# Kernel tuning notes

Hardware: AMD Instinct MI355X
Metric: run time of the kernel (lower is better)

The kernel has to match this reference:

```python
import jax, jax.numpy as jnp
import numpy as np

B, C, H, W = 4, 256, 64, 64
HID = max(C // 8, 64)  # = 64


def setup_inputs() -> dict:
    key = jax.random.key(0)
    ks = jax.random.split(key, 8)
    s_in = 1.0 / np.sqrt(C)
    return {
        "x1": jax.random.normal(ks[0], (B, C, H, W), dtype=jnp.float32),
        "x2": jax.random.normal(ks[1], (B, C, H, W), dtype=jnp.float32),
        "Wq": jax.random.normal(ks[2], (HID, C), dtype=jnp.float32) * s_in,
        "bq": jnp.zeros((HID,), dtype=jnp.float32),
        "Wk": jax.random.normal(ks[3], (HID, C), dtype=jnp.float32) * s_in,
        "bk": jnp.zeros((HID,), dtype=jnp.float32),
        "Wv": jax.random.normal(ks[4], (C, C), dtype=jnp.float32) * s_in,
        "bv": jnp.zeros((C,), dtype=jnp.float32),
        "gamma": jnp.ones((1,), dtype=jnp.float32) * 0.5,  # nonzero so attention path matters
    }


def _conv1x1(x, Wt, b):
    # 1x1 conv == per-pixel GEMM: (O,C) x (B,C,H,W) -> (B,O,H,W)
    return jnp.einsum("oc,bchw->bohw", Wt, x) + b[None, :, None, None]


def _cross_attend(xq, xkv, Wq, bq, Wk, bk, Wv, bv, gamma):
    b, c, h, w = xq.shape
    n = h * w
    q = _conv1x1(xq, Wq, bq).reshape(b, -1, n)    # (B, hid, N)
    k = _conv1x1(xkv, Wk, bk).reshape(b, -1, n)   # (B, hid, N)
    v = _conv1x1(xkv, Wv, bv).reshape(b, c, n)    # (B, C, N)
    # attn[b,n,m] = softmax_m( q[:, :, n] . k[:, :, m] )
    attn = jax.nn.softmax(jnp.einsum("bhn,bhm->bnm", q, k), axis=-1)
    out = jnp.einsum("bcm,bnm->bcn", v, attn).reshape(b, c, h, w)
    return xq + gamma[0] * out


def reference(x1, x2, Wq, bq, Wk, bk, Wv, bv, gamma):
    x1_att = _cross_attend(x1, x2, Wq, bq, Wk, bk, Wv, bv, gamma)
    x2_att = _cross_attend(x2, x1, Wq, bq, Wk, bk, Wv, bv, gamma)
    return (x1_att, x2_att)
```

## Files before the change

kernel.cpp:

```cpp
#include <hip/hip_runtime.h>
#include <hip/hip_bf16.h>

#define NPIX 4096
#define CCH  256
#define HID  64
#define BAT  4
#define XSTR 264
#define PTS  136


using f32x4 = __attribute__((ext_vector_type(4))) float;
using h16x8 = __attribute__((ext_vector_type(8))) _Float16;
using u16x4 = __attribute__((ext_vector_type(4))) unsigned short;

#define L2E 1.44269504088896340736f

__device__ __forceinline__ unsigned short f2h(float f) {
    _Float16 h = (_Float16)f;
    return __builtin_bit_cast(unsigned short, h);
}
__device__ __forceinline__ h16x8 ldg_fragh(const unsigned short* p) {
    uint4 v = *reinterpret_cast<const uint4*>(p);
    return __builtin_bit_cast(h16x8, v);
}
__device__ __forceinline__ h16x8 lds_fragh(const unsigned short* p) {
    return *reinterpret_cast<const h16x8*>(p);
}
__device__ __forceinline__ unsigned int pk2h(float a, float b) {
    auto t = __builtin_amdgcn_cvt_pkrtz(a, b);
    return __builtin_bit_cast(unsigned int, t);
}
__device__ __forceinline__ float sel4(float a0, float a1, float a2, float a3, int q) {
    float x = (q & 1) ? a1 : a0;
    float y = (q & 1) ? a3 : a2;
    return (q & 2) ? y : x;
}

__global__ __launch_bounds__(256, 1) void wcvt_kernel(
    const float* __restrict__ Wq, const float* __restrict__ Wk,
    const float* __restrict__ Wv, unsigned short* __restrict__ Wg)
{
    int tid = blockIdx.x * 256 + threadIdx.x;
    int tile = tid >> 6, lane = tid & 63;
    int r = (tile >> 3) * 16 + (lane & 15);
    int c = (tile & 7) * 32 + (lane >> 4) * 8;
    const float* src; float sc;
    if (r < 64)       { src = Wq + r * CCH + c;        sc = L2E; }
    else if (r < 128) { src = Wk + (r - 64) * CCH + c; sc = 1.0f; }
    else              { src = Wv + (r - 128) * CCH + c; sc = 1.0f; }
    float4 a = *reinterpret_cast<const float4*>(src);
    float4 b4 = *reinterpret_cast<const float4*>(src + 4);
    uint4 out;
    out.x = pk2h(a.x * sc, a.y * sc);
    out.y = pk2h(a.z * sc, a.w * sc);
    out.z = pk2h(b4.x * sc, b4.y * sc);
    out.w = pk2h(b4.z * sc, b4.w * sc);
    *reinterpret_cast<uint4*>(Wg + tile * 512 + lane * 8) = out;
}

__global__ __launch_bounds__(256, 2) void proj_kernel(
    const float* __restrict__ x1, const float* __restrict__ x2,
    const unsigned short* __restrict__ Wg,
    const float* __restrict__ bq, const float* __restrict__ bk,
    const float* __restrict__ bv,
    unsigned short* __restrict__ Qf, unsigned short* __restrict__ Kf,
    unsigned short* __restrict__ Vt)
{
    __shared__ unsigned short xs[32][XSTR];

    const int Lb = blockIdx.x;
    const int sb = Lb & 7;
    const int tile = Lb >> 3;
    const int s = sb >> 2, b = sb & 3;
    const float* x = s ? x2 : x1;
    const int n0 = tile * 32;
    const int t = threadIdx.x;
    const int lane = t & 63;
    const int w = __builtin_amdgcn_readfirstlane(t >> 6);
    const int quad = lane >> 4, lq = lane & 15;

    {
        const int n = t & 31;
        const int g = t >> 5;
        const float* xb = x + (size_t)(b * CCH) * NPIX + n0;
        #pragma unroll
        for (int i = 0; i < 8; ++i) {
            int c0 = g * 4 + i * 32;
            u16x4 hv;
            #pragma unroll
            for (int j = 0; j < 4; ++j)
                hv[j] = f2h(xb[(size_t)(c0 + j) * NPIX + n]);
            *reinterpret_cast<u16x4*>(&xs[n][c0]) = hv;
        }
    }
    __syncthreads();

    h16x8 xf[2][8];
    #pragma unroll
    for (int nt = 0; nt < 2; ++nt)
        #pragma unroll
        for (int ks = 0; ks < 8; ++ks)
            xf[nt][ks] = lds_fragh(&xs[nt * 16 + lq][ks * 32 + quad * 8]);

    unsigned short* Qb = Qf + (size_t)(s * BAT + b) * (NPIX * HID);
    unsigned short* Kb = Kf + (size_t)(s * BAT + b) * (NPIX * HID);
    unsigned short* Vb = Vt + (size_t)(s * BAT + b) * ((size_t)CCH * NPIX);

    h16x8 wf[2][8];
    {
        const unsigned short* wp = Wg + (size_t)(w * 6 * 8) * 512 + lane * 8;
        #pragma unroll
        for (int ks = 0; ks < 8; ++ks) wf[0][ks] = ldg_fragh(wp + ks * 512);
    }

    #pragma unroll
    for (int hloop = 0; hloop < 6; ++hloop) {
        const int cur = hloop & 1;
        const int idx = w * 6 + hloop;
        const int kind = idx < 4 ? 0 : (idx < 8 ? 1 : 2);

        if (hloop < 5) {
            const unsigned short* wp = Wg + (size_t)((idx + 1) * 8) * 512 + lane * 8;
            #pragma unroll
            for (int ks = 0; ks < 8; ++ks) wf[cur ^ 1][ks] = ldg_fragh(wp + ks * 512);
        }

        if (kind == 2) {
            const int cbase = (idx - 8) * 16;
            const float bbv = bv[cbase + lq];
            #pragma unroll
            for (int nt = 0; nt < 2; ++nt) {
                f32x4 acc = (f32x4){0.f, 0.f, 0.f, 0.f};
                #pragma unroll
                for (int ks = 0; ks < 8; ++ks)
                    acc = __builtin_amdgcn_mfma_f32_16x16x32_f16(xf[nt][ks], wf[cur][ks], acc, 0, 0, 0);
                u16x4 pk;
                #pragma unroll
                for (int reg = 0; reg < 4; ++reg) pk[reg] = f2h(acc[reg] + bbv);
                size_t off = (size_t)((idx - 8) * 128 + (n0 >> 5)) * 512
                           + (nt * 2 + (quad >> 1)) * 128 + lq * 8 + (quad & 1) * 4;
                *reinterpret_cast<unsigned long long*>(Vb + off) =
                    __builtin_bit_cast(unsigned long long, pk);
            }
        } else {
            unsigned short* dq = (kind ? Kb : Qb);
            const float* bias = (kind ? bk : bq);
            const float scl = kind ? 1.0f : L2E;
            const int hb16 = kind ? (idx - 4) : idx;
            float bb4[4];
            #pragma unroll
            for (int reg = 0; reg < 4; ++reg)
                bb4[reg] = bias[hb16 * 16 + quad * 4 + reg] * scl;
            #pragma unroll
            for (int nt = 0; nt < 2; ++nt) {
                f32x4 acc = (f32x4){0.f, 0.f, 0.f, 0.f};
                #pragma unroll
                for (int ks = 0; ks < 8; ++ks)
                    acc = __builtin_amdgcn_mfma_f32_16x16x32_f16(wf[cur][ks], xf[nt][ks], acc, 0, 0, 0);
                u16x4 pk;
                #pragma unroll
                for (int reg = 0; reg < 4; ++reg) pk[reg] = f2h(acc[reg] + bb4[reg]);
                size_t off = (size_t)((n0 >> 4) + nt) * 1024 + (hb16 >> 1) * 512
                           + ((hb16 & 1) * 2 + (quad >> 1)) * 128 + lq * 8 + (quad & 1) * 4;
                *reinterpret_cast<unsigned long long*>(dq + off) =
                    __builtin_bit_cast(unsigned long long, pk);
            }
        }
    }
}

__global__ __launch_bounds__(256, 2) void smax_kernel(
    const unsigned short* __restrict__ Qf, const unsigned short* __restrict__ Kf,
    float* __restrict__ Mg)
{
    __shared__ float Msh[4][64];

    const int Lb = blockIdx.x;
    const int g = Lb & 7;
    const int ntile = Lb >> 3;
    const int d = g >> 2, b = g & 3;
    const int db = d * BAT + b;
    const int s = d, r = 1 - d;
    const int n0 = ntile * 64;

    const int t = threadIdx.x;
    const int lane = t & 63;
    const int w = __builtin_amdgcn_readfirstlane(t >> 6);
    const int quad = lane >> 4, lq = lane & 15;

    const unsigned short* Qb = Qf + (size_t)(s * BAT + b) * (NPIX * HID);
    const unsigned short* Kb = Kf + (size_t)(r * BAT + b) * (NPIX * HID);

    h16x8 qf[4][2];
    #pragma unroll
    for (int nt = 0; nt < 4; ++nt)
        #pragma unroll
        for (int ks = 0; ks < 2; ++ks)
            qf[nt][ks] = ldg_fragh(Qb + (size_t)((((n0 >> 4) + nt) * 2) + ks) * 512 + lane * 8);

    float mx[4] = {-3.0e38f, -3.0e38f, -3.0e38f, -3.0e38f};

    h16x8 kfA[2][2], kfB[2][2];

#define SMAX_LOAD(BUF, IT)                                                      \
    {                                                                           \
        _Pragma("unroll")                                                       \
        for (int mt = 0; mt < 2; ++mt) {                                        \
            _Pragma("unroll")                                                   \
            for (int ks = 0; ks < 2; ++ks)                                      \
                BUF[mt][ks] = ldg_fragh(                                        \
                    Kb + (size_t)(((IT) * 8 + w * 2 + mt) * 2 + ks) * 512       \
                       + lane * 8);                                             \
        }                                                                       \
    }
#define SMAX_STEP(BUF)                                                          \
    {                                                                           \
        f32x4 Sacc[2][4];                                                       \
        _Pragma("unroll")                                                       \
        for (int mt = 0; mt < 2; ++mt) {                                        \
            _Pragma("unroll")                                                   \
            for (int nt = 0; nt < 4; ++nt)                                      \
                Sacc[mt][nt] = (f32x4){0.f, 0.f, 0.f, 0.f};                     \
        }                                                                       \
        _Pragma("unroll")                                                       \
        for (int mt = 0; mt < 2; ++mt) {                                        \
            _Pragma("unroll")                                                   \
            for (int ks = 0; ks < 2; ++ks) {                                    \
                _Pragma("unroll")                                               \
                for (int nt = 0; nt < 4; ++nt)                                  \
                    Sacc[mt][nt] = __builtin_amdgcn_mfma_f32_16x16x32_f16(      \
                        BUF[mt][ks], qf[nt][ks], Sacc[mt][nt], 0, 0, 0);        \
            }                                                                   \
        }                                                                       \
        _Pragma("unroll")                                                       \
        for (int mt = 0; mt < 2; ++mt) {                                        \
            _Pragma("unroll")                                                   \
            for (int nt = 0; nt < 4; ++nt)                                      \
                mx[nt] = fmaxf(mx[nt],                                          \
                    fmaxf(fmaxf(Sacc[mt][nt][0], Sacc[mt][nt][1]),              \
                          fmaxf(Sacc[mt][nt][2], Sacc[mt][nt][3])));            \
        }                                                                       \
    }

    SMAX_LOAD(kfA, 0)
    for (int it = 0; it < 32; it += 2) {
        if (it + 1 < 32) SMAX_LOAD(kfB, it + 1)
        SMAX_STEP(kfA)
        if (it + 2 < 32) SMAX_LOAD(kfA, it + 2)
        SMAX_STEP(kfB)
    }
#undef SMAX_LOAD
#undef SMAX_STEP

    #pragma unroll
    for (int nt = 0; nt < 4; ++nt) {
        mx[nt] = fmaxf(mx[nt], __shfl_xor(mx[nt], 16));
        mx[nt] = fmaxf(mx[nt], __shfl_xor(mx[nt], 32));
    }
    Msh[w][quad * 16 + lq] = sel4(mx[0], mx[1], mx[2], mx[3], quad);
    __syncthreads();

    if (t < 64) {
        float m = fmaxf(fmaxf(Msh[0][t], Msh[1][t]), fmaxf(Msh[2][t], Msh[3][t]));
        Mg[(size_t)db * NPIX + n0 + t] = m;
    }
}

__global__ __launch_bounds__(256, 2) void attn_kernel(
    const float* __restrict__ x1, const float* __restrict__ x2,
    const unsigned short* __restrict__ Qf, const unsigned short* __restrict__ Kf,
    const unsigned short* __restrict__ Vt,
    const float* __restrict__ Mg, const float* __restrict__ gamma,
    float* __restrict__ out)
{
    __shared__ unsigned short PT[2][64 * PTS];
    __shared__ float Lsh[4][64];

    const int Lb = blockIdx.x;
    const int g = Lb & 7;
    const int ntile = Lb >> 3;
    const int d = g >> 2, b = g & 3;
    const int db = d * BAT + b;
    const int s = d, r = 1 - d;
    const int n0 = ntile * 64;

    const int t = threadIdx.x;
    const int lane = t & 63;
    const int w = __builtin_amdgcn_readfirstlane(t >> 6);
    const int quad = lane >> 4, lq = lane & 15;

    const unsigned short* Qb = Qf + (size_t)(s * BAT + b) * (NPIX * HID);
    const unsigned short* Kb = Kf + (size_t)(r * BAT + b) * (NPIX * HID);
    const unsigned short* Vb = Vt + (size_t)(r * BAT + b) * ((size_t)CCH * NPIX);

    float Mn[4];
    #pragma unroll
    for (int nt = 0; nt < 4; ++nt)
        Mn[nt] = Mg[(size_t)db * NPIX + n0 + nt * 16 + lq];

    h16x8 qf[4][2];
    #pragma unroll
    for (int nt = 0; nt < 4; ++nt)
        #pragma unroll
        for (int ks = 0; ks < 2; ++ks)
            qf[nt][ks] = ldg_fragh(Qb + (size_t)((((n0 >> 4) + nt) * 2) + ks) * 512 + lane * 8);

    f32x4 Oacc[4][4];
    #pragma unroll
    for (int rt = 0; rt < 4; ++rt)
        #pragma unroll
        for (int ct = 0; ct < 4; ++ct)
            Oacc[rt][ct] = (f32x4){0.f, 0.f, 0.f, 0.f};

    float Li[4] = {0.f, 0.f, 0.f, 0.f};

    h16x8 kf[2][2];
    #pragma unroll
    for (int mt = 0; mt < 2; ++mt)
        #pragma unroll
        for (int ks = 0; ks < 2; ++ks)
            kf[mt][ks] = ldg_fragh(Kb + (size_t)((w * 2 + mt) * 2 + ks) * 512 + lane * 8);

    h16x8 vf[4][4];
    #pragma unroll
    for (int ks = 0; ks < 4; ++ks)
        #pragma unroll
        for (int rt = 0; rt < 4; ++rt)
            vf[ks][rt] = ldg_fragh(Vb + (size_t)((w * 4 + rt) * 128 + ks) * 512 + lane * 8);

    for (int it = 0; it < 32; ++it) {
        const int buf = it & 1;

        f32x4 Sacc[2][4];
        #pragma unroll
        for (int mt = 0; mt < 2; ++mt)
            #pragma unroll
            for (int nt = 0; nt < 4; ++nt)
                Sacc[mt][nt] = (f32x4){-Mn[nt], -Mn[nt], -Mn[nt], -Mn[nt]};
        #pragma unroll
        for (int mt = 0; mt < 2; ++mt)
            #pragma unroll
            for (int ks = 0; ks < 2; ++ks)
                #pragma unroll
                for (int nt = 0; nt < 4; ++nt)
                    Sacc[mt][nt] = __builtin_amdgcn_mfma_f32_16x16x32_f16(
                        kf[mt][ks], qf[nt][ks], Sacc[mt][nt], 0, 0, 0);

        const int itk = (it < 31) ? it + 1 : 31;
        #pragma unroll
        for (int mt = 0; mt < 2; ++mt)
            #pragma unroll
            for (int ks = 0; ks < 2; ++ks)
                kf[mt][ks] = ldg_fragh(Kb + (size_t)((itk * 8 + w * 2 + mt) * 2 + ks) * 512
                                          + lane * 8);

        #pragma unroll
        for (int mt = 0; mt < 2; ++mt)
            #pragma unroll
            for (int nt = 0; nt < 4; ++nt) {
                float p0 = __builtin_amdgcn_exp2f(Sacc[mt][nt][0]);
                float p1 = __builtin_amdgcn_exp2f(Sacc[mt][nt][1]);
                float p2 = __builtin_amdgcn_exp2f(Sacc[mt][nt][2]);
                float p3 = __builtin_amdgcn_exp2f(Sacc[mt][nt][3]);
                Li[nt] += (p0 + p1) + (p2 + p3);
                uint2 pk2;
                pk2.x = pk2h(p0, p1);
                pk2.y = pk2h(p2, p3);
                *reinterpret_cast<uint2*>(
                    &PT[buf][(nt * 16 + lq) * PTS + w * 32 + mt * 16 + quad * 4]) = pk2;
            }
        __syncthreads();

        #pragma unroll
        for (int ks = 0; ks < 4; ++ks) {
            h16x8 pf[4];
            #pragma unroll
            for (int ct = 0; ct < 4; ++ct)
                pf[ct] = lds_fragh(&PT[buf][(ct * 16 + lq) * PTS + ks * 32 + quad * 8]);
            #pragma unroll
            for (int rt = 0; rt < 4; ++rt)
                #pragma unroll
                for (int ct = 0; ct < 4; ++ct)
                    Oacc[rt][ct] = __builtin_amdgcn_mfma_f32_16x16x32_f16(
                        vf[ks][rt], pf[ct], Oacc[rt][ct], 0, 0, 0);
        }

        const int itv = (it < 31) ? it + 1 : 31;
        #pragma unroll
        for (int ks = 0; ks < 4; ++ks)
            #pragma unroll
            for (int rt = 0; rt < 4; ++rt)
                vf[ks][rt] = ldg_fragh(Vb + (size_t)((w * 4 + rt) * 128 + itv * 4 + ks) * 512
                                          + lane * 8);
    }

    #pragma unroll
    for (int nt = 0; nt < 4; ++nt) {
        Li[nt] += __shfl_xor(Li[nt], 16);
        Li[nt] += __shfl_xor(Li[nt], 32);
    }
    Lsh[w][quad * 16 + lq] = sel4(Li[0], Li[1], Li[2], Li[3], quad);
    __syncthreads();

    float inv[4];
    #pragma unroll
    for (int nt = 0; nt < 4; ++nt) {
        int i = nt * 16 + lq;
        inv[nt] = 1.0f / ((Lsh[0][i] + Lsh[1][i]) + (Lsh[2][i] + Lsh[3][i]));
    }

    const float* xq = d ? x2 : x1;
    const float gm = gamma[0];

    #pragma unroll
    for (int rt = 0; rt < 4; ++rt)
        #pragma unroll
        for (int ct = 0; ct < 4; ++ct)
            #pragma unroll
            for (int rg = 0; rg < 4; ++rg) {
                int c = w * 64 + rt * 16 + quad * 4 + rg;
                int nn = n0 + ct * 16 + lq;
                size_t src = (size_t)(b * CCH + c) * NPIX + nn;
                size_t dst = (size_t)(db * CCH + c) * NPIX + nn;
                out[dst] = xq[src] + gm * Oacc[rt][ct][rg] * inv[ct];
            }
}

extern "C" void kernel_launch(void* const* d_in, const int* in_sizes, int n_in,
                              void* d_out, int out_size, void* d_ws, size_t ws_size,
                              hipStream_t stream) {
    (void)in_sizes; (void)n_in; (void)out_size; (void)ws_size;
    const float* x1 = (const float*)d_in[0];
    const float* x2 = (const float*)d_in[1];
    const float* Wq = (const float*)d_in[2];
    const float* bq = (const float*)d_in[3];
    const float* Wk = (const float*)d_in[4];
    const float* bk = (const float*)d_in[5];
    const float* Wv = (const float*)d_in[6];
    const float* bv = (const float*)d_in[7];
    const float* gm = (const float*)d_in[8];
    float* out = (float*)d_out;

    unsigned short* ws = (unsigned short*)d_ws;
    unsigned short* Qf = ws;
    unsigned short* Kf = Qf + (size_t)2097152;
    unsigned short* Vt = Kf + (size_t)2097152;
    unsigned short* Wg = Vt + (size_t)8388608;
    float* Mg = (float*)(Wg + 98304);

    wcvt_kernel<<<dim3(48), dim3(256), 0, stream>>>(Wq, Wk, Wv, Wg);
    proj_kernel<<<dim3(1024), dim3(256), 0, stream>>>(
        x1, x2, Wg, bq, bk, bv, Qf, Kf, Vt);
    smax_kernel<<<dim3(512), dim3(256), 0, stream>>>(Qf, Kf, Mg);
    attn_kernel<<<dim3(512), dim3(256), 0, stream>>>(
        x1, x2, Qf, Kf, Vt, Mg, gm, out);
}
```

Baseline: 208.6 us.

## Replace separate row-max pass with lazy online softmax rescaling in attention

Removes the smax_kernel, which recomputed the full QK^T to find exact row maxima, and instead tracks a running max inside attn_kernel. Rescaling of the accumulators and row sums happens only when a tile's logits exceed the current max by more than a threshold. This saves one full QK^T pass and a kernel launch. In exchange it adds a per-iteration cross-wave max reduction through shared memory plus an extra __syncthreads, and unnormalized exponentials may grow up to 2^8 in fp16 before a rescale.

```diff
diff --git a/kernel.cpp b/kernel.cpp
--- a/kernel.cpp
+++ b/kernel.cpp
@@ -7,6 +7,7 @@
 #define BAT  4
 #define XSTR 264
 #define PTS  136
+#define RTHR 8.0f
 
 
 using f32x4 = __attribute__((ext_vector_type(4))) float;
@@ -169,11 +170,15 @@
     }
 }
 
-__global__ __launch_bounds__(256, 2) void smax_kernel(
+__global__ __launch_bounds__(256, 2) void attn_kernel(
+    const float* __restrict__ x1, const float* __restrict__ x2,
     const unsigned short* __restrict__ Qf, const unsigned short* __restrict__ Kf,
-    float* __restrict__ Mg)
+    const unsigned short* __restrict__ Vt,
+    const float* __restrict__ gamma, float* __restrict__ out)
 {
-    __shared__ float Msh[4][64];
+    __shared__ unsigned short PT[2][64 * PTS];
+    __shared__ float Lsh[4][64];
+    __shared__ float Tsh[4][64];
 
     const int Lb = blockIdx.x;
     const int g = Lb & 7;
@@ -190,6 +195,7 @@
 
     const unsigned short* Qb = Qf + (size_t)(s * BAT + b) * (NPIX * HID);
     const unsigned short* Kb = Kf + (size_t)(r * BAT + b) * (NPIX * HID);
+    const unsigned short* Vb = Vt + (size_t)(r * BAT + b) * ((size_t)CCH * NPIX);
 
     h16x8 qf[4][2];
     #pragma unroll
@@ -198,113 +204,6 @@
         for (int ks = 0; ks < 2; ++ks)
             qf[nt][ks] = ldg_fragh(Qb + (size_t)((((n0 >> 4) + nt) * 2) + ks) * 512 + lane * 8);
 
-    float mx[4] = {-3.0e38f, -3.0e38f, -3.0e38f, -3.0e38f};
-
-    h16x8 kfA[2][2], kfB[2][2];
-
-#define SMAX_LOAD(BUF, IT)                                                      \
-    {                                                                           \
-        _Pragma("unroll")                                                       \
-        for (int mt = 0; mt < 2; ++mt) {                                        \
-            _Pragma("unroll")                                                   \
-            for (int ks = 0; ks < 2; ++ks)                                      \
-                BUF[mt][ks] = ldg_fragh(                                        \
-                    Kb + (size_t)(((IT) * 8 + w * 2 + mt) * 2 + ks) * 512       \
-                       + lane * 8);                                             \
-        }                                                                       \
-    }
-#define SMAX_STEP(BUF)                                                          \
-    {                                                                           \
-        f32x4 Sacc[2][4];                                                       \
-        _Pragma("unroll")                                                       \
-        for (int mt = 0; mt < 2; ++mt) {                                        \
-            _Pragma("unroll")                                                   \
-            for (int nt = 0; nt < 4; ++nt)                                      \
-                Sacc[mt][nt] = (f32x4){0.f, 0.f, 0.f, 0.f};                     \
-        }                                                                       \
-        _Pragma("unroll")                                                       \
-        for (int mt = 0; mt < 2; ++mt) {                                        \
-            _Pragma("unroll")                                                   \
-            for (int ks = 0; ks < 2; ++ks) {                                    \
-                _Pragma("unroll")                                               \
-                for (int nt = 0; nt < 4; ++nt)                                  \
-                    Sacc[mt][nt] = __builtin_amdgcn_mfma_f32_16x16x32_f16(      \
-                        BUF[mt][ks], qf[nt][ks], Sacc[mt][nt], 0, 0, 0);        \
-            }                                                                   \
-        }                                                                       \
-        _Pragma("unroll")                                                       \
-        for (int mt = 0; mt < 2; ++mt) {                                        \
-            _Pragma("unroll")                                                   \
-            for (int nt = 0; nt < 4; ++nt)                                      \
-                mx[nt] = fmaxf(mx[nt],                                          \
-                    fmaxf(fmaxf(Sacc[mt][nt][0], Sacc[mt][nt][1]),              \
-                          fmaxf(Sacc[mt][nt][2], Sacc[mt][nt][3])));            \
-        }                                                                       \
-    }
-
-    SMAX_LOAD(kfA, 0)
-    for (int it = 0; it < 32; it += 2) {
-        if (it + 1 < 32) SMAX_LOAD(kfB, it + 1)
-        SMAX_STEP(kfA)
-        if (it + 2 < 32) SMAX_LOAD(kfA, it + 2)
-        SMAX_STEP(kfB)
-    }
-#undef SMAX_LOAD
-#undef SMAX_STEP
-
-    #pragma unroll
-    for (int nt = 0; nt < 4; ++nt) {
-        mx[nt] = fmaxf(mx[nt], __shfl_xor(mx[nt], 16));
-        mx[nt] = fmaxf(mx[nt], __shfl_xor(mx[nt], 32));
-    }
-    Msh[w][quad * 16 + lq] = sel4(mx[0], mx[1], mx[2], mx[3], quad);
-    __syncthreads();
-
-    if (t < 64) {
-        float m = fmaxf(fmaxf(Msh[0][t], Msh[1][t]), fmaxf(Msh[2][t], Msh[3][t]));
-        Mg[(size_t)db * NPIX + n0 + t] = m;
-    }
-}
-
-__global__ __launch_bounds__(256, 2) void attn_kernel(
-    const float* __restrict__ x1, const float* __restrict__ x2,
-    const unsigned short* __restrict__ Qf, const unsigned short* __restrict__ Kf,
-    const unsigned short* __restrict__ Vt,
-    const float* __restrict__ Mg, const float* __restrict__ gamma,
-    float* __restrict__ out)
-{
-    __shared__ unsigned short PT[2][64 * PTS];
-    __shared__ float Lsh[4][64];
-
-    const int Lb = blockIdx.x;
-    const int g = Lb & 7;
-    const int ntile = Lb >> 3;
-    const int d = g >> 2, b = g & 3;
-    const int db = d * BAT + b;
-    const int s = d, r = 1 - d;
-    const int n0 = ntile * 64;
-
-    const int t = threadIdx.x;
-    const int lane = t & 63;
-    const int w = __builtin_amdgcn_readfirstlane(t >> 6);
-    const int quad = lane >> 4, lq = lane & 15;
-
-    const unsigned short* Qb = Qf + (size_t)(s * BAT + b) * (NPIX * HID);
-    const unsigned short* Kb = Kf + (size_t)(r * BAT + b) * (NPIX * HID);
-    const unsigned short* Vb = Vt + (size_t)(r * BAT + b) * ((size_t)CCH * NPIX);
-
-    float Mn[4];
-    #pragma unroll
-    for (int nt = 0; nt < 4; ++nt)
-        Mn[nt] = Mg[(size_t)db * NPIX + n0 + nt * 16 + lq];
-
-    h16x8 qf[4][2];
-    #pragma unroll
-    for (int nt = 0; nt < 4; ++nt)
-        #pragma unroll
-        for (int ks = 0; ks < 2; ++ks)
-            qf[nt][ks] = ldg_fragh(Qb + (size_t)((((n0 >> 4) + nt) * 2) + ks) * 512 + lane * 8);
-
     f32x4 Oacc[4][4];
     #pragma unroll
     for (int rt = 0; rt < 4; ++rt)
@@ -313,6 +212,7 @@
             Oacc[rt][ct] = (f32x4){0.f, 0.f, 0.f, 0.f};
 
     float Li[4] = {0.f, 0.f, 0.f, 0.f};
+    float Mv[4] = {0.f, 0.f, 0.f, 0.f};
 
     h16x8 kf[2][2];
     #pragma unroll
@@ -336,7 +236,7 @@
         for (int mt = 0; mt < 2; ++mt)
             #pragma unroll
             for (int nt = 0; nt < 4; ++nt)
-                Sacc[mt][nt] = (f32x4){-Mn[nt], -Mn[nt], -Mn[nt], -Mn[nt]};
+                Sacc[mt][nt] = (f32x4){-Mv[nt], -Mv[nt], -Mv[nt], -Mv[nt]};
         #pragma unroll
         for (int mt = 0; mt < 2; ++mt)
             #pragma unroll
@@ -353,6 +253,49 @@
             for (int ks = 0; ks < 2; ++ks)
                 kf[mt][ks] = ldg_fragh(Kb + (size_t)((itk * 8 + w * 2 + mt) * 2 + ks) * 512
                                           + lane * 8);
+
+        float trel[4];
+        #pragma unroll
+        for (int nt = 0; nt < 4; ++nt) {
+            float ta = fmaxf(fmaxf(Sacc[0][nt][0], Sacc[0][nt][1]),
+                             fmaxf(Sacc[0][nt][2], Sacc[0][nt][3]));
+            float tb = fmaxf(fmaxf(Sacc[1][nt][0], Sacc[1][nt][1]),
+                             fmaxf(Sacc[1][nt][2], Sacc[1][nt][3]));
+            float tm = fmaxf(ta, tb);
+            tm = fmaxf(tm, __shfl_xor(tm, 16));
+            tm = fmaxf(tm, __shfl_xor(tm, 32));
+            trel[nt] = tm;
+        }
+        Tsh[w][quad * 16 + lq] = sel4(trel[0], trel[1], trel[2], trel[3], quad);
+        __syncthreads();
+
+        float bm[4];
+        #pragma unroll
+        for (int nt = 0; nt < 4; ++nt) {
+            int i = nt * 16 + lq;
+            bm[nt] = fmaxf(fmaxf(Tsh[0][i], Tsh[1][i]),
+                           fmaxf(Tsh[2][i], Tsh[3][i]));
+        }
+        if (__any((bm[0] > RTHR) || (bm[1] > RTHR) ||
+                  (bm[2] > RTHR) || (bm[3] > RTHR))) {
+            #pragma unroll
+            for (int nt = 0; nt < 4; ++nt) {
+                float dlt = fmaxf(bm[nt], 0.f);
+                float sc = __builtin_amdgcn_exp2f(-dlt);
+                Mv[nt] += dlt;
+                Li[nt] *= sc;
+                #pragma unroll
+                for (int mt = 0; mt < 2; ++mt)
+                    #pragma unroll
+                    for (int rg = 0; rg < 4; ++rg)
+                        Sacc[mt][nt][rg] -= dlt;
+                #pragma unroll
+                for (int rt = 0; rt < 4; ++rt)
+                    #pragma unroll
+                    for (int rg = 0; rg < 4; ++rg)
+                        Oacc[rt][nt][rg] *= sc;
+            }
+        }
 
         #pragma unroll
         for (int mt = 0; mt < 2; ++mt)
@@ -446,12 +389,10 @@
     unsigned short* Kf = Qf + (size_t)2097152;
     unsigned short* Vt = Kf + (size_t)2097152;
     unsigned short* Wg = Vt + (size_t)8388608;
-    float* Mg = (float*)(Wg + 98304);
 
     wcvt_kernel<<<dim3(48), dim3(256), 0, stream>>>(Wq, Wk, Wv, Wg);
     proj_kernel<<<dim3(1024), dim3(256), 0, stream>>>(
         x1, x2, Wg, bq, bk, bv, Qf, Kf, Vt);
-    smax_kernel<<<dim3(512), dim3(256), 0, stream>>>(Qf, Kf, Mg);
     attn_kernel<<<dim3(512), dim3(256), 0, stream>>>(
-        x1, x2, Qf, Kf, Vt, Mg, gm, out);
-}
+        x1, x2, Qf, Kf, Vt, gm, out);
+}
```

New measurement: 193.8 us. 7.1% less time.
